# Performance work log

Hardware: AMD Instinct MI355X
Metric: run time of the kernel (lower is better)

## Reference

```python
import jax, jax.numpy as jnp
import numpy as np

STRIDES = (8, 16, 32)
INPUT = (640, 640)
NC = 80           # num_classes
CONF = 0.65       # conf_thr
IOU_THR = 0.65    # nms iou_threshold
K = 1000          # fixed candidate cap for jit-compatible NMS (padded/masked)


def _priors():
    # MlvlPointGenerator(offset=0, with_stride=True): per level, points at
    # (x*stride, y*stride) flattened y-major, format [cx, cy, stride, stride].
    ps = []
    for s in STRIDES:
        H, W = INPUT[0] // s, INPUT[1] // s
        yy, xx = jnp.meshgrid(jnp.arange(H, dtype=jnp.float32),
                              jnp.arange(W, dtype=jnp.float32), indexing='ij')
        cx = (xx * s).ravel()
        cy = (yy * s).ravel()
        st = jnp.full_like(cx, float(s))
        ps.append(jnp.stack([cx, cy, st, st], axis=-1))
    return jnp.concatenate(ps, axis=0)  # [8400, 4]


def _flatten(xs, c):
    # permute(0,2,3,1).reshape(B, -1, c) per level, concat over priors
    return jnp.concatenate(
        [x.transpose(0, 2, 3, 1).reshape(x.shape[0], -1, c) for x in xs], axis=1)


def _decode(priors, bp):
    # bp: [B, N, 4]; priors: [N, 4] (cx, cy, sw, sh)
    xys = bp[..., :2] * priors[:, 2:] + priors[:, :2]
    whs = jnp.exp(bp[..., 2:]) * priors[:, 2:]
    tl = xys - whs * 0.5
    br = xys + whs * 0.5
    return jnp.concatenate([tl, br], axis=-1)  # [B, N, 4] tlbr


def _iou(a, b):
    tl = jnp.maximum(a[:, None, :2], b[None, :, :2])
    br = jnp.minimum(a[:, None, 2:], b[None, :, 2:])
    wh = jnp.clip(br - tl, 0.0)
    inter = wh[..., 0] * wh[..., 1]
    area = lambda x: (x[:, 2] - x[:, 0]) * (x[:, 3] - x[:, 1])
    union = area(a)[:, None] + area(b)[None, :] - inter
    return inter / (union + 1e-6)


def _nms_single(cls_s, obj_s, boxes):
    # cls_s: [N, NC] sigmoid scores; obj_s: [N]; boxes: [N, 4]
    max_s = cls_s.max(axis=-1)
    labels = jnp.argmax(cls_s, axis=-1)
    score = max_s * obj_s
    valid = score >= CONF                       # confidence mask
    sc = jnp.where(valid, score, 0.0)
    top_sc, idx = jax.lax.top_k(sc, K)          # sorted descending -> greedy order
    b = boxes[idx]
    lab = labels[idx]
    v = valid[idx]
    # class-aware (batched) NMS: offset boxes per label so classes never overlap
    max_coord = jnp.max(jnp.abs(b)) + 1.0
    ob = b + (lab.astype(b.dtype) * max_coord)[:, None]
    iou = _iou(ob, ob)                          # [K, K]
    j = jnp.arange(K)
    def body(i, keep):
        sup = (iou[i] > IOU_THR) & (j > i)
        return jnp.where(keep[i] & v[i], keep & (~sup), keep)
    keep = jax.lax.fori_loop(0, K, body, jnp.ones(K, dtype=bool))
    final = keep & v
    dets = jnp.where(final[:, None],
                     jnp.concatenate([b, top_sc[:, None]], axis=-1), 0.0)  # [K, 5]
    labs = jnp.where(final, lab, -1)
    return dets, labs, final


def setup_inputs() -> dict:
    key = jax.random.key(0)
    ks = jax.random.split(key, 9)
    B = 32
    shapes = {
        'cls0': (B, NC, 80, 80), 'cls1': (B, NC, 40, 40), 'cls2': (B, NC, 20, 20),
        'bbox0': (B, 4, 80, 80), 'bbox1': (B, 4, 40, 40), 'bbox2': (B, 4, 20, 20),
        'obj0': (B, 1, 80, 80), 'obj1': (B, 1, 40, 40), 'obj2': (B, 1, 20, 20),
    }
    return {n: jax.random.normal(k, s, dtype=jnp.float32)
            for (n, s), k in zip(shapes.items(), ks)}


def reference(cls0, cls1, cls2, bbox0, bbox1, bbox2, obj0, obj1, obj2):
    priors = _priors()
    cls = jax.nn.sigmoid(_flatten([cls0, cls1, cls2], NC))       # [B, 8400, 80]
    bp = _flatten([bbox0, bbox1, bbox2], 4)                      # [B, 8400, 4]
    obj = jax.nn.sigmoid(_flatten([obj0, obj1, obj2], 1)[..., 0])  # [B, 8400]
    boxes = _decode(priors, bp)                                  # [B, 8400, 4]
    # per-image class-wise batched NMS, padded to K detections
    dets, labels, keep = jax.vmap(_nms_single)(cls, obj, boxes)
    return dets, labels, keep
```

## Files before the change

kernel.cpp:

```cpp
#include <hip/hip_runtime.h>
#include <stdint.h>

#define NPRIOR 8400
#define NB 32
#define NCLS 80
#define KTOP 1000
#define CAP 8400
#define CPAD 16

typedef unsigned long long u64;

__device__ __forceinline__ float exp_np(float x) {
#pragma clang fp contract(off)
    if (x > 88.72283935546875f) return __builtin_huge_valf();
    if (x < -87.3365478515625f) return 0.0f;
    float q = rintf(x * 1.442695040f);
    float r = fmaf(q, -6.93145752e-1f, x);
    r = fmaf(q, -1.42860677e-6f, r);
    float p = fmaf(1.9875691500e-4f, r, 1.3981999507e-3f);
    p = fmaf(p, r, 8.3334519073e-3f);
    p = fmaf(p, r, 4.1665795894e-2f);
    p = fmaf(p, r, 1.6666665459e-1f);
    p = fmaf(p, r, 5.0000001201e-1f);
    float r2 = r * r;
    p = fmaf(p, r2, r);
    p = p + 1.0f;
    return ldexpf(p, (int)q);
}
__device__ __forceinline__ float sigm_np(float x) {
#pragma clang fp contract(off)
    float t = exp_np(-x);
    return 1.0f / (1.0f + t);
}

__device__ __forceinline__ void level_of(int n, int& W, int& s, int& loc) {
    if (n < 6400)      { W = 80; s = 8;  loc = n; }
    else if (n < 8000) { W = 40; s = 16; loc = n - 6400; }
    else               { W = 20; s = 32; loc = n - 8000; }
}

__device__ float4 decode32(int b, int n,
                           const float* bb0, const float* bb1, const float* bb2) {
#pragma clang fp contract(off)
    int W, s, loc; level_of(n, W, s, loc);
    const float* bb = (s == 8) ? bb0 : (s == 16) ? bb1 : bb2;
    int hw = W * W;
    int y = loc / W, x = loc - y * W;
    const float* bp = bb + (size_t)b * 4 * hw + y * W + x;
    float fs = (float)s;
    float cx = (float)x * fs, cy = (float)y * fs;
    float xc = bp[0] * fs + cx;
    float yc = bp[hw] * fs + cy;
    float wv = exp_np(bp[2 * hw]) * fs;
    float hv = exp_np(bp[3 * hw]) * fs;
    float wv2 = wv * 0.5f, hv2 = hv * 0.5f;
    float4 r;
    r.x = xc - wv2;
    r.y = yc - hv2;
    r.z = xc + wv2;
    r.w = yc + hv2;
    return r;
}

__device__ __forceinline__ unsigned flt2ord(float f) {
    unsigned u = __float_as_uint(f);
    return u ^ ((u >> 31) ? 0xffffffffu : 0x80000000u);
}
__device__ __forceinline__ float ord2flt(unsigned u) {
    u ^= ((u >> 31) ? 0x80000000u : 0xffffffffu);
    return __uint_as_float(u);
}
__device__ __forceinline__ u64 packlc(float l, int c) {
    return ((u64)flt2ord(l) << 32) | (unsigned)(~(unsigned)c);
}

__global__ void __launch_bounds__(64) init_k(int* __restrict__ cnts_mb) {
    cnts_mb[threadIdx.x * CPAD] = 0;
}

__global__ void __launch_bounds__(256) score_k(
    const float* __restrict__ cls0, const float* __restrict__ cls1, const float* __restrict__ cls2,
    const float* __restrict__ ob0,  const float* __restrict__ ob1,  const float* __restrict__ ob2,
    float* __restrict__ sc, int* __restrict__ labels,
    u64* __restrict__ keys, int* __restrict__ cnts, int* __restrict__ rankbuf)
{
#pragma clang fp contract(off)
    int b = blockIdx.y;
    int tid = threadIdx.x, wv = tid >> 6, l = tid & 63;
    int cid = l >> 4;
    int n = blockIdx.x * 64 + wv * 16 + (l & 15);
    bool nvalid = (n < NPRIOR);
    int nc = nvalid ? n : NPRIOR - 1;
    int W, s, loc; level_of(nc, W, s, loc);
    const float* cls = (s == 8) ? cls0 : (s == 16) ? cls1 : cls2;
    const float* ob  = (s == 8) ? ob0  : (s == 16) ? ob1  : ob2;
    int hw = W * W;
    int y = loc / W, x = loc - y * W;
    const float* cp = cls + (size_t)b * NCLS * hw + y * W + x;
    int c0 = cid * 20;

    float buf[20];
#pragma unroll
    for (int k = 0; k < 20; ++k) buf[k] = cp[(size_t)(c0 + k) * hw];
    float M = buf[0], S2 = -3.4e38f;
    int I = c0;
#pragma unroll
    for (int k = 1; k < 20; ++k) {
        float lg = buf[k];
        if (lg > M) { S2 = M; M = lg; I = c0 + k; }
        else        { S2 = fmaxf(S2, lg); }
    }
    u64 p = packlc(M, I);
    float s2 = S2;
#pragma unroll
    for (int mk = 16; mk <= 32; mk <<= 1) {
        u64 po = __shfl_xor(p, mk, 64);
        float so = __shfl_xor(s2, mk, 64);
        if (po > p) { s2 = fmaxf(so, ord2flt((unsigned)(p >> 32))); p = po; }
        else        { s2 = fmaxf(s2, ord2flt((unsigned)(po >> 32))); }
    }

    float Mg = ord2flt((unsigned)(p >> 32));
    int lab = (int)(~(unsigned)(p & 0xffffffffull)) & 0xff;
    float tM = sigm_np(Mg);
    float gap = Mg - s2;
    float mx = fmaxf(fabsf(Mg), fabsf(s2));
    bool need = !((gap * exp_np(-mx)) > 1.6e-5f) && nvalid;
    if (__ballot(need)) {
        u64 pk = 0;
#pragma unroll
        for (int k = 0; k < 20; ++k) {
            float t = sigm_np(cp[(size_t)(c0 + k) * hw]);
            u64 q = ((u64)flt2ord(t) << 32) | (unsigned)(~(unsigned)(c0 + k));
            pk = (q > pk) ? q : pk;
        }
#pragma unroll
        for (int mk = 16; mk <= 32; mk <<= 1) {
            u64 qo = __shfl_xor(pk, mk, 64);
            pk = (qo > pk) ? qo : pk;
        }
        if (need) {
            tM = ord2flt((unsigned)(pk >> 32));
            lab = (int)(~(unsigned)(pk & 0xffffffffull)) & 0xff;
        }
    }

    bool owner = (cid == 0) && nvalid;
    float scv = 0.0f;
    if (owner) {
        float sObj = sigm_np(ob[(size_t)b * hw + y * W + x]);
        float score = tM * sObj;
        scv = (score >= 0.65f) ? score : 0.0f;
        sc[(size_t)b * NPRIOR + n] = scv;
        labels[(size_t)b * NPRIOR + n] = lab;
    }

    bool val = owner && (scv > 0.0f);
    u64 mb = __ballot(val);
    if (mb) {
        int lead = (int)__builtin_ctzll(mb);
        int base = 0;
        if (l == lead) base = atomicAdd(&cnts[b * CPAD], (int)__popcll(mb));
        base = __shfl(base, lead);
        if (val) {
            int pos = base + (int)__popcll(mb & ((1ull << l) - 1ull));
            keys[(size_t)b * CAP + pos] =
                ((u64)__float_as_uint(scv) << 32) | (unsigned)(~(unsigned)n);
            rankbuf[(size_t)b * CAP + pos] = 0;
        }
    }
}

__global__ void __launch_bounds__(256) rank_part(
    const u64* __restrict__ keys, const int* __restrict__ cnts,
    int* __restrict__ rankbuf)
{
    int b = blockIdx.y, tid = threadIdx.x;
    int cn = min(cnts[b * CPAD], CAP);
    int nt = (cn + 255) >> 8;
    int ntt = nt * nt;
    const u64* keyimg = keys + (size_t)b * CAP;
    int lane = tid & 63;

    for (int t = blockIdx.x; t < ntt; t += gridDim.x) {
        int it = t / nt, jt = t - it * nt;
        int i = it * 256 + tid;
        u64 ki = (i < cn) ? keyimg[i] : ~0ull;
        int rank = 0;
        int jbase = jt * 256;
        int jend = min(jbase + 256, cn);
        for (int jb = jbase; jb < jend; jb += 64) {
            int j = jb + lane;
            u64 kv = (j < cn) ? keyimg[j] : 0ull;
            unsigned lo = (unsigned)kv, hi = (unsigned)(kv >> 32);
            int lim = jend - jb;
#pragma unroll
            for (int l = 0; l < 64; ++l) {
                unsigned jlo = __builtin_amdgcn_readlane(lo, l);
                unsigned jhi = __builtin_amdgcn_readlane(hi, l);
                u64 kj = ((u64)jhi << 32) | jlo;
                rank += (l < lim && kj > ki) ? 1 : 0;
            }
        }
        if (i < cn && rank > 0) atomicAdd(&rankbuf[(size_t)b * CAP + i], rank);
    }
}

__global__ void __launch_bounds__(256) scatter_k(
    const u64* __restrict__ keys, const int* __restrict__ cnts,
    const int* __restrict__ rankbuf,
    const float* __restrict__ sc, const int* __restrict__ labels,
    const float* __restrict__ bb0, const float* __restrict__ bb1, const float* __restrict__ bb2,
    float4* __restrict__ sel_box, float* __restrict__ sel_score,
    int* __restrict__ sel_label, int* __restrict__ maxbits, u64* __restrict__ vmask)
{
#pragma clang fp contract(off)
    __shared__ float redbuf[256];
    int b = blockIdx.y, chunk = blockIdx.x, tid = threadIdx.x;
    int cn = min(cnts[b * CPAD], CAP);
    int base = chunk * 256;
    if (chunk != 0 && base >= cn) return;

    const u64* keyimg = keys + (size_t)b * CAP;
    const int* labb = labels + (size_t)b * NPRIOR;
    const float* scb = sc + (size_t)b * NPRIOR;

    int i = base + tid;
    float lmax = 0.0f;
    if (i < cn) {
        int rank = rankbuf[(size_t)b * CAP + i];
        if (rank < KTOP) {
            u64 ki = keyimg[i];
            unsigned n = ~(unsigned)(ki & 0xffffffffull);
            float s = __uint_as_float((unsigned)(ki >> 32));
            float4 bx = decode32(b, (int)n, bb0, bb1, bb2);
            sel_box[(size_t)b * 1024 + rank] = bx;
            sel_score[(size_t)b * 1024 + rank] = s;
            sel_label[(size_t)b * 1024 + rank] = labb[n];
            lmax = fmaxf(fmaxf(fabsf(bx.x), fabsf(bx.y)),
                         fmaxf(fabsf(bx.z), fabsf(bx.w)));
        }
    }

    if (chunk == 0) {
        if (cn < KTOP && tid == 0) {
            float lm = 0.0f;
            int r = cn;
            for (int n = 0; n < NPRIOR && r < KTOP; ++n) {
                if (scb[n] == 0.0f) {
                    float4 bx = decode32(b, n, bb0, bb1, bb2);
                    sel_box[(size_t)b * 1024 + r] = bx;
                    sel_score[(size_t)b * 1024 + r] = 0.0f;
                    sel_label[(size_t)b * 1024 + r] = labb[n];
                    lm = fmaxf(lm, fmaxf(fmaxf(fabsf(bx.x), fabsf(bx.y)),
                                         fmaxf(fabsf(bx.z), fabsf(bx.w))));
                    ++r;
                }
            }
            lmax = fmaxf(lmax, lm);
        }
        if (tid < 24) {
            sel_box[(size_t)b * 1024 + 1000 + tid] = make_float4(0.f, 0.f, 0.f, 0.f);
            sel_score[(size_t)b * 1024 + 1000 + tid] = 0.0f;
            sel_label[(size_t)b * 1024 + 1000 + tid] = 0;
        }
        if (tid < 16) {
            int vc = min(cn, KTOP);
            int lo = tid * 64;
            u64 m;
            if (vc >= lo + 64)      m = ~0ull;
            else if (vc <= lo)      m = 0ull;
            else                    m = (1ull << (vc - lo)) - 1ull;
            vmask[b * 16 + tid] = m;
        }
    }

    redbuf[tid] = lmax;
    __syncthreads();
    for (int off = 128; off > 0; off >>= 1) {
        if (tid < off) redbuf[tid] = fmaxf(redbuf[tid], redbuf[tid + off]);
        __syncthreads();
    }
    if (tid == 0) atomicMax(&maxbits[b * CPAD], __float_as_int(redbuf[0]));
}

__global__ void __launch_bounds__(256) build_mask_T(
    const float4* __restrict__ sel_box, const int* __restrict__ sel_label,
    const int* __restrict__ maxbits, u64* __restrict__ Cmask)
{
#pragma clang fp contract(off)
    __shared__ float4 obr[256];
    __shared__ float arr[256];
    int b = blockIdx.y;
    int cg = blockIdx.x & 15, rgq = blockIdx.x >> 4;
    if (rgq * 4 > cg) return;
    int tid = threadIdx.x, wave = tid >> 6, lane = tid & 63;
    float mc = __int_as_float(maxbits[b * CPAD]) + 1.0f;

    {
        int row = rgq * 256 + tid;
        float4 v = sel_box[(size_t)b * 1024 + row];
        float off = (float)sel_label[(size_t)b * 1024 + row] * mc;
        v.x += off; v.y += off; v.z += off; v.w += off;
        obr[tid] = v;
        arr[tid] = (v.z - v.x) * (v.w - v.y);
    }
    int col = cg * 64 + lane;
    float4 a = sel_box[(size_t)b * 1024 + col];
    float offc = (float)sel_label[(size_t)b * 1024 + col] * mc;
    a.x += offc; a.y += offc; a.z += offc; a.w += offc;
    float ac = (a.z - a.x) * (a.w - a.y);
    __syncthreads();

    int rg = rgq * 4 + wave;
    if (rg > cg) return;
    u64 bits = 0;
    int rowbase = rg * 64;
#pragma unroll 8
    for (int r = 0; r < 64; ++r) {
        int row = rowbase + r;
        float4 rb = obr[wave * 64 + r];
        float ra = arr[wave * 64 + r];
        bool pred = false;
        if (row < col && row < KTOP && col < KTOP) {
            float tlx = fmaxf(rb.x, a.x), tly = fmaxf(rb.y, a.y);
            float brx = fminf(rb.z, a.z), bry = fminf(rb.w, a.w);
            float w = fmaxf(brx - tlx, 0.0f), h = fmaxf(bry - tly, 0.0f);
            float inter = w * h;
            float uni = (ra + ac) - inter;
            float iou = inter / (uni + 1e-6f);
            pred = iou > 0.65f;
        }
        bits |= pred ? (1ull << r) : 0ull;
    }
    Cmask[((size_t)b * 16 + rg) * 1024 + col] = bits;
}

__global__ void __launch_bounds__(64) nms_fixpoint_write(
    const u64* __restrict__ Cmask, const u64* __restrict__ vmask,
    const float4* __restrict__ sel_box, const float* __restrict__ sel_score,
    const int* __restrict__ sel_label, float* __restrict__ out)
{
    int b = blockIdx.x, lane = threadIdx.x;
    const u64* Cimg = Cmask + (size_t)b * 16 * 1024;
    u64 Khist[16];
#pragma unroll
    for (int g = 0; g < 16; ++g) {
        int col = g * 64 + lane;
        bool supp = false;
#pragma unroll
        for (int gp = 0; gp < g; ++gp)
            supp |= (Cimg[(size_t)gp * 1024 + col] & Khist[gp]) != 0ull;
        u64 V = vmask[b * 16 + g] & ~__ballot(supp);
        u64 T = Cimg[(size_t)g * 1024 + col];
        u64 K = V;
        for (int it = 0; it < 64; ++it) {
            u64 Knew = V & ~__ballot((T & K) != 0ull);
            if (Knew == K) break;
            K = Knew;
        }
        Khist[g] = K;
    }

    const size_t selo = (size_t)b * 1024;
    float* lab_o = out + (size_t)NB * KTOP * 5;
    float* keep_o = lab_o + (size_t)NB * KTOP;
#pragma unroll
    for (int g = 0; g < 16; ++g) {
        int k = g * 64 + lane;
        if (k >= KTOP) break;
        bool fin = (Khist[g] >> lane) & 1ull;
        float4 bx = sel_box[selo + k];
        float s = sel_score[selo + k];
        int lb = sel_label[selo + k];
        size_t o5 = ((size_t)b * KTOP + k) * 5;
        out[o5 + 0] = fin ? bx.x : 0.0f;
        out[o5 + 1] = fin ? bx.y : 0.0f;
        out[o5 + 2] = fin ? bx.z : 0.0f;
        out[o5 + 3] = fin ? bx.w : 0.0f;
        out[o5 + 4] = fin ? s : 0.0f;
        lab_o[b * KTOP + k] = fin ? (float)lb : -1.0f;
        keep_o[b * KTOP + k] = fin ? 1.0f : 0.0f;
    }
}

extern "C" void kernel_launch(void* const* d_in, const int* in_sizes, int n_in,
                              void* d_out, int out_size, void* d_ws, size_t ws_size,
                              hipStream_t stream) {
    const float* cls0 = (const float*)d_in[0];
    const float* cls1 = (const float*)d_in[1];
    const float* cls2 = (const float*)d_in[2];
    const float* bb0  = (const float*)d_in[3];
    const float* bb1  = (const float*)d_in[4];
    const float* bb2  = (const float*)d_in[5];
    const float* ob0  = (const float*)d_in[6];
    const float* ob1  = (const float*)d_in[7];
    const float* ob2  = (const float*)d_in[8];
    float* out = (float*)d_out;

    char* w = (char*)d_ws;
    size_t used = 0;
    auto alloc = [&](size_t bytes) -> void* {
        void* p = (void*)(w + used);
        used += (bytes + 255) & ~(size_t)255;
        return p;
    };
    float* sc        = (float*)alloc((size_t)NB * NPRIOR * 4);
    int* labels      = (int*)alloc((size_t)NB * NPRIOR * 4);
    u64* keys        = (u64*)alloc((size_t)NB * CAP * 8);
    int* cnts_mb     = (int*)alloc((size_t)2 * NB * CPAD * 4);
    int* rankbuf     = (int*)alloc((size_t)NB * CAP * 4);
    float4* sel_box  = (float4*)alloc((size_t)NB * 1024 * 16);
    float* sel_score = (float*)alloc((size_t)NB * 1024 * 4);
    int* sel_label   = (int*)alloc((size_t)NB * 1024 * 4);
    u64* vmask       = (u64*)alloc((size_t)NB * 16 * 8);
    u64* Cmask       = (u64*)alloc((size_t)NB * 16 * 1024 * 8);

    if (used > ws_size) return;

    int* cnts = cnts_mb;
    int* maxbits = cnts_mb + NB * CPAD;

    init_k<<<1, 64, 0, stream>>>(cnts_mb);
    score_k<<<dim3((NPRIOR + 63) / 64, NB), 256, 0, stream>>>(
        cls0, cls1, cls2, ob0, ob1, ob2, sc, labels, keys, cnts, rankbuf);
    rank_part<<<dim3(64, NB), 256, 0, stream>>>(keys, cnts, rankbuf);
    scatter_k<<<dim3((CAP + 255) / 256, NB), 256, 0, stream>>>(
        keys, cnts, rankbuf, sc, labels, bb0, bb1, bb2,
        sel_box, sel_score, sel_label, maxbits, vmask);
    build_mask_T<<<dim3(64, NB), 256, 0, stream>>>(sel_box, sel_label, maxbits, Cmask);
    nms_fixpoint_write<<<NB, 64, 0, stream>>>(
        Cmask, vmask, sel_box, sel_score, sel_label, out);
}
```

Before: 117.4 us.

## Fuse rank, scatter, mask-build and NMS into one persistent kernel with grid barriers

Replaces four separate kernel launches (rank, scatter, IoU mask build, fixpoint NMS) with a single persistent kernel of 512 blocks that loops over the work items of each stage and uses software grid-wide barriers between stages. The init kernel is replaced by a hipMemsetAsync that also zeroes the barrier counters. This removes launch gaps and per-kernel tail effects. In exchange it relies on all 512 blocks being co-resident, since a spin barrier otherwise deadlocks or times out, and the final NMS stage runs on only 32 blocks while the rest sit idle.

Result: slower. 345.1 us (+193.8%).

```diff
diff --git a/kernel.cpp b/kernel.cpp
--- a/kernel.cpp
+++ b/kernel.cpp
@@ -7,6 +7,7 @@
 #define KTOP 1000
 #define CAP 8400
 #define CPAD 16
+#define FBLK 512
 
 typedef unsigned long long u64;
 
@@ -74,10 +75,6 @@
     return ((u64)flt2ord(l) << 32) | (unsigned)(~(unsigned)c);
 }
 
-__global__ void __launch_bounds__(64) init_k(int* __restrict__ cnts_mb) {
-    cnts_mb[threadIdx.x * CPAD] = 0;
-}
-
 __global__ void __launch_bounds__(256) score_k(
     const float* __restrict__ cls0, const float* __restrict__ cls1, const float* __restrict__ cls2,
     const float* __restrict__ ob0,  const float* __restrict__ ob1,  const float* __restrict__ ob2,
@@ -171,216 +168,233 @@
     }
 }
 
-__global__ void __launch_bounds__(256) rank_part(
-    const u64* __restrict__ keys, const int* __restrict__ cnts,
-    int* __restrict__ rankbuf)
-{
-    int b = blockIdx.y, tid = threadIdx.x;
-    int cn = min(cnts[b * CPAD], CAP);
-    int nt = (cn + 255) >> 8;
-    int ntt = nt * nt;
-    const u64* keyimg = keys + (size_t)b * CAP;
-    int lane = tid & 63;
-
-    for (int t = blockIdx.x; t < ntt; t += gridDim.x) {
-        int it = t / nt, jt = t - it * nt;
-        int i = it * 256 + tid;
-        u64 ki = (i < cn) ? keyimg[i] : ~0ull;
-        int rank = 0;
-        int jbase = jt * 256;
-        int jend = min(jbase + 256, cn);
-        for (int jb = jbase; jb < jend; jb += 64) {
-            int j = jb + lane;
-            u64 kv = (j < cn) ? keyimg[j] : 0ull;
-            unsigned lo = (unsigned)kv, hi = (unsigned)(kv >> 32);
-            int lim = jend - jb;
-#pragma unroll
-            for (int l = 0; l < 64; ++l) {
-                unsigned jlo = __builtin_amdgcn_readlane(lo, l);
-                unsigned jhi = __builtin_amdgcn_readlane(hi, l);
-                u64 kj = ((u64)jhi << 32) | jlo;
-                rank += (l < lim && kj > ki) ? 1 : 0;
-            }
-        }
-        if (i < cn && rank > 0) atomicAdd(&rankbuf[(size_t)b * CAP + i], rank);
-    }
-}
-
-__global__ void __launch_bounds__(256) scatter_k(
-    const u64* __restrict__ keys, const int* __restrict__ cnts,
-    const int* __restrict__ rankbuf,
+__device__ __forceinline__ void gridbar(int* bar, int slot) {
+    __syncthreads();
+    if (threadIdx.x == 0) {
+        __threadfence();
+        int* cnt = bar + slot * 2;
+        int* rel = bar + slot * 2 + 1;
+        int prev = __hip_atomic_fetch_add(cnt, 1, __ATOMIC_ACQ_REL, __HIP_MEMORY_SCOPE_AGENT);
+        if (prev == FBLK - 1) {
+            __hip_atomic_store(rel, 1, __ATOMIC_RELEASE, __HIP_MEMORY_SCOPE_AGENT);
+        } else {
+            long spins = 0;
+            while (__hip_atomic_load(rel, __ATOMIC_ACQUIRE, __HIP_MEMORY_SCOPE_AGENT) == 0) {
+                if (++spins > 300000000L) break;
+                __builtin_amdgcn_s_sleep(8);
+            }
+        }
+        __threadfence();
+    }
+    __syncthreads();
+}
+
+__global__ void __launch_bounds__(256, 4) fused_k(
+    const u64* __restrict__ keys, int* __restrict__ cnts,
+    int* __restrict__ rankbuf,
     const float* __restrict__ sc, const int* __restrict__ labels,
     const float* __restrict__ bb0, const float* __restrict__ bb1, const float* __restrict__ bb2,
     float4* __restrict__ sel_box, float* __restrict__ sel_score,
-    int* __restrict__ sel_label, int* __restrict__ maxbits, u64* __restrict__ vmask)
-{
-#pragma clang fp contract(off)
-    __shared__ float redbuf[256];
-    int b = blockIdx.y, chunk = blockIdx.x, tid = threadIdx.x;
-    int cn = min(cnts[b * CPAD], CAP);
-    int base = chunk * 256;
-    if (chunk != 0 && base >= cn) return;
-
-    const u64* keyimg = keys + (size_t)b * CAP;
-    const int* labb = labels + (size_t)b * NPRIOR;
-    const float* scb = sc + (size_t)b * NPRIOR;
-
-    int i = base + tid;
-    float lmax = 0.0f;
-    if (i < cn) {
-        int rank = rankbuf[(size_t)b * CAP + i];
-        if (rank < KTOP) {
-            u64 ki = keyimg[i];
-            unsigned n = ~(unsigned)(ki & 0xffffffffull);
-            float s = __uint_as_float((unsigned)(ki >> 32));
-            float4 bx = decode32(b, (int)n, bb0, bb1, bb2);
-            sel_box[(size_t)b * 1024 + rank] = bx;
-            sel_score[(size_t)b * 1024 + rank] = s;
-            sel_label[(size_t)b * 1024 + rank] = labb[n];
-            lmax = fmaxf(fmaxf(fabsf(bx.x), fabsf(bx.y)),
-                         fmaxf(fabsf(bx.z), fabsf(bx.w)));
-        }
-    }
-
-    if (chunk == 0) {
-        if (cn < KTOP && tid == 0) {
-            float lm = 0.0f;
-            int r = cn;
-            for (int n = 0; n < NPRIOR && r < KTOP; ++n) {
-                if (scb[n] == 0.0f) {
-                    float4 bx = decode32(b, n, bb0, bb1, bb2);
-                    sel_box[(size_t)b * 1024 + r] = bx;
-                    sel_score[(size_t)b * 1024 + r] = 0.0f;
-                    sel_label[(size_t)b * 1024 + r] = labb[n];
-                    lm = fmaxf(lm, fmaxf(fmaxf(fabsf(bx.x), fabsf(bx.y)),
-                                         fmaxf(fabsf(bx.z), fabsf(bx.w))));
-                    ++r;
-                }
-            }
-            lmax = fmaxf(lmax, lm);
-        }
-        if (tid < 24) {
-            sel_box[(size_t)b * 1024 + 1000 + tid] = make_float4(0.f, 0.f, 0.f, 0.f);
-            sel_score[(size_t)b * 1024 + 1000 + tid] = 0.0f;
-            sel_label[(size_t)b * 1024 + 1000 + tid] = 0;
-        }
-        if (tid < 16) {
-            int vc = min(cn, KTOP);
-            int lo = tid * 64;
-            u64 m;
-            if (vc >= lo + 64)      m = ~0ull;
-            else if (vc <= lo)      m = 0ull;
-            else                    m = (1ull << (vc - lo)) - 1ull;
-            vmask[b * 16 + tid] = m;
-        }
-    }
-
-    redbuf[tid] = lmax;
-    __syncthreads();
-    for (int off = 128; off > 0; off >>= 1) {
-        if (tid < off) redbuf[tid] = fmaxf(redbuf[tid], redbuf[tid + off]);
-        __syncthreads();
-    }
-    if (tid == 0) atomicMax(&maxbits[b * CPAD], __float_as_int(redbuf[0]));
-}
-
-__global__ void __launch_bounds__(256) build_mask_T(
-    const float4* __restrict__ sel_box, const int* __restrict__ sel_label,
-    const int* __restrict__ maxbits, u64* __restrict__ Cmask)
+    int* __restrict__ sel_label, int* __restrict__ maxbits, u64* __restrict__ vmask,
+    u64* __restrict__ Cmask, float* __restrict__ out, int* __restrict__ bar)
 {
 #pragma clang fp contract(off)
     __shared__ float4 obr[256];
     __shared__ float arr[256];
-    int b = blockIdx.y;
-    int cg = blockIdx.x & 15, rgq = blockIdx.x >> 4;
-    if (rgq * 4 > cg) return;
-    int tid = threadIdx.x, wave = tid >> 6, lane = tid & 63;
-    float mc = __int_as_float(maxbits[b * CPAD]) + 1.0f;
-
-    {
-        int row = rgq * 256 + tid;
-        float4 v = sel_box[(size_t)b * 1024 + row];
-        float off = (float)sel_label[(size_t)b * 1024 + row] * mc;
-        v.x += off; v.y += off; v.z += off; v.w += off;
-        obr[tid] = v;
-        arr[tid] = (v.z - v.x) * (v.w - v.y);
-    }
-    int col = cg * 64 + lane;
-    float4 a = sel_box[(size_t)b * 1024 + col];
-    float offc = (float)sel_label[(size_t)b * 1024 + col] * mc;
-    a.x += offc; a.y += offc; a.z += offc; a.w += offc;
-    float ac = (a.z - a.x) * (a.w - a.y);
-    __syncthreads();
-
-    int rg = rgq * 4 + wave;
-    if (rg > cg) return;
-    u64 bits = 0;
-    int rowbase = rg * 64;
+    __shared__ float redbuf[256];
+    int blk = blockIdx.x, tid = threadIdx.x, lane = tid & 63;
+
+    for (int j = blk; j < NB * 64; j += FBLK) {
+        int b = j >> 6, slot = j & 63;
+        int cn = min(cnts[b * CPAD], CAP);
+        int nt = (cn + 255) >> 8;
+        int ntt = nt * nt;
+        const u64* keyimg = keys + (size_t)b * CAP;
+        for (int t = slot; t < ntt; t += 64) {
+            int it = t / nt, jt = t - it * nt;
+            int i = it * 256 + tid;
+            u64 ki = (i < cn) ? keyimg[i] : ~0ull;
+            int rank = 0;
+            int jbase = jt * 256;
+            int jend = min(jbase + 256, cn);
+            for (int jb = jbase; jb < jend; jb += 64) {
+                int jj = jb + lane;
+                u64 kv = (jj < cn) ? keyimg[jj] : 0ull;
+                unsigned lo = (unsigned)kv, hi = (unsigned)(kv >> 32);
+                int lim = jend - jb;
+#pragma unroll
+                for (int l2 = 0; l2 < 64; ++l2) {
+                    unsigned jlo = __builtin_amdgcn_readlane(lo, l2);
+                    unsigned jhi = __builtin_amdgcn_readlane(hi, l2);
+                    u64 kj = ((u64)jhi << 32) | jlo;
+                    rank += (l2 < lim && kj > ki) ? 1 : 0;
+                }
+            }
+            if (i < cn && rank > 0) atomicAdd(&rankbuf[(size_t)b * CAP + i], rank);
+        }
+    }
+    gridbar(bar, 0);
+
+    for (int j = blk; j < NB * 33; j += FBLK) {
+        int b = j / 33, chunk = j - b * 33;
+        int cn = min(cnts[b * CPAD], CAP);
+        int base = chunk * 256;
+        if (chunk != 0 && base >= cn) continue;
+
+        const u64* keyimg = keys + (size_t)b * CAP;
+        const int* labb = labels + (size_t)b * NPRIOR;
+        const float* scb = sc + (size_t)b * NPRIOR;
+
+        int i = base + tid;
+        float lmax = 0.0f;
+        if (i < cn) {
+            int rank = rankbuf[(size_t)b * CAP + i];
+            if (rank < KTOP) {
+                u64 ki = keyimg[i];
+                unsigned n = ~(unsigned)(ki & 0xffffffffull);
+                float s = __uint_as_float((unsigned)(ki >> 32));
+                float4 bx = decode32(b, (int)n, bb0, bb1, bb2);
+                sel_box[(size_t)b * 1024 + rank] = bx;
+                sel_score[(size_t)b * 1024 + rank] = s;
+                sel_label[(size_t)b * 1024 + rank] = labb[n];
+                lmax = fmaxf(fmaxf(fabsf(bx.x), fabsf(bx.y)),
+                             fmaxf(fabsf(bx.z), fabsf(bx.w)));
+            }
+        }
+        if (chunk == 0) {
+            if (cn < KTOP && tid == 0) {
+                float lm = 0.0f;
+                int r = cn;
+                for (int n = 0; n < NPRIOR && r < KTOP; ++n) {
+                    if (scb[n] == 0.0f) {
+                        float4 bx = decode32(b, n, bb0, bb1, bb2);
+                        sel_box[(size_t)b * 1024 + r] = bx;
+                        sel_score[(size_t)b * 1024 + r] = 0.0f;
+                        sel_label[(size_t)b * 1024 + r] = labb[n];
+                        lm = fmaxf(lm, fmaxf(fmaxf(fabsf(bx.x), fabsf(bx.y)),
+                                             fmaxf(fabsf(bx.z), fabsf(bx.w))));
+                        ++r;
+                    }
+                }
+                lmax = fmaxf(lmax, lm);
+            }
+            if (tid < 24) {
+                sel_box[(size_t)b * 1024 + 1000 + tid] = make_float4(0.f, 0.f, 0.f, 0.f);
+                sel_score[(size_t)b * 1024 + 1000 + tid] = 0.0f;
+                sel_label[(size_t)b * 1024 + 1000 + tid] = 0;
+            }
+            if (tid < 16) {
+                int vc = min(cn, KTOP);
+                int lo = tid * 64;
+                u64 m;
+                if (vc >= lo + 64)      m = ~0ull;
+                else if (vc <= lo)      m = 0ull;
+                else                    m = (1ull << (vc - lo)) - 1ull;
+                vmask[b * 16 + tid] = m;
+            }
+        }
+        __syncthreads();
+        redbuf[tid] = lmax;
+        __syncthreads();
+        for (int off = 128; off > 0; off >>= 1) {
+            if (tid < off) redbuf[tid] = fmaxf(redbuf[tid], redbuf[tid + off]);
+            __syncthreads();
+        }
+        if (tid == 0) atomicMax(&maxbits[b * CPAD], __float_as_int(redbuf[0]));
+    }
+    gridbar(bar, 1);
+
+    for (int j = blk; j < NB * 64; j += FBLK) {
+        int b = j >> 6, xx = j & 63;
+        int cg = xx & 15, rgq = xx >> 4;
+        if (rgq * 4 > cg) continue;
+        int wave = tid >> 6;
+        float mc = __int_as_float(
+            __hip_atomic_load(&maxbits[b * CPAD], __ATOMIC_RELAXED,
+                              __HIP_MEMORY_SCOPE_AGENT)) + 1.0f;
+        __syncthreads();
+        {
+            int row = rgq * 256 + tid;
+            float4 v = sel_box[(size_t)b * 1024 + row];
+            float off = (float)sel_label[(size_t)b * 1024 + row] * mc;
+            v.x += off; v.y += off; v.z += off; v.w += off;
+            obr[tid] = v;
+            arr[tid] = (v.z - v.x) * (v.w - v.y);
+        }
+        int col = cg * 64 + lane;
+        float4 a = sel_box[(size_t)b * 1024 + col];
+        float offc = (float)sel_label[(size_t)b * 1024 + col] * mc;
+        a.x += offc; a.y += offc; a.z += offc; a.w += offc;
+        float ac = (a.z - a.x) * (a.w - a.y);
+        __syncthreads();
+
+        int rg = rgq * 4 + wave;
+        if (rg <= cg) {
+            u64 bits = 0;
+            int rowbase = rg * 64;
 #pragma unroll 8
-    for (int r = 0; r < 64; ++r) {
-        int row = rowbase + r;
-        float4 rb = obr[wave * 64 + r];
-        float ra = arr[wave * 64 + r];
-        bool pred = false;
-        if (row < col && row < KTOP && col < KTOP) {
-            float tlx = fmaxf(rb.x, a.x), tly = fmaxf(rb.y, a.y);
-            float brx = fminf(rb.z, a.z), bry = fminf(rb.w, a.w);
-            float w = fmaxf(brx - tlx, 0.0f), h = fmaxf(bry - tly, 0.0f);
-            float inter = w * h;
-            float uni = (ra + ac) - inter;
-            float iou = inter / (uni + 1e-6f);
-            pred = iou > 0.65f;
-        }
-        bits |= pred ? (1ull << r) : 0ull;
-    }
-    Cmask[((size_t)b * 16 + rg) * 1024 + col] = bits;
-}
-
-__global__ void __launch_bounds__(64) nms_fixpoint_write(
-    const u64* __restrict__ Cmask, const u64* __restrict__ vmask,
-    const float4* __restrict__ sel_box, const float* __restrict__ sel_score,
-    const int* __restrict__ sel_label, float* __restrict__ out)
-{
-    int b = blockIdx.x, lane = threadIdx.x;
-    const u64* Cimg = Cmask + (size_t)b * 16 * 1024;
-    u64 Khist[16];
-#pragma unroll
-    for (int g = 0; g < 16; ++g) {
-        int col = g * 64 + lane;
-        bool supp = false;
-#pragma unroll
-        for (int gp = 0; gp < g; ++gp)
-            supp |= (Cimg[(size_t)gp * 1024 + col] & Khist[gp]) != 0ull;
-        u64 V = vmask[b * 16 + g] & ~__ballot(supp);
-        u64 T = Cimg[(size_t)g * 1024 + col];
-        u64 K = V;
-        for (int it = 0; it < 64; ++it) {
-            u64 Knew = V & ~__ballot((T & K) != 0ull);
-            if (Knew == K) break;
-            K = Knew;
-        }
-        Khist[g] = K;
-    }
-
-    const size_t selo = (size_t)b * 1024;
-    float* lab_o = out + (size_t)NB * KTOP * 5;
-    float* keep_o = lab_o + (size_t)NB * KTOP;
-#pragma unroll
-    for (int g = 0; g < 16; ++g) {
-        int k = g * 64 + lane;
-        if (k >= KTOP) break;
-        bool fin = (Khist[g] >> lane) & 1ull;
-        float4 bx = sel_box[selo + k];
-        float s = sel_score[selo + k];
-        int lb = sel_label[selo + k];
-        size_t o5 = ((size_t)b * KTOP + k) * 5;
-        out[o5 + 0] = fin ? bx.x : 0.0f;
-        out[o5 + 1] = fin ? bx.y : 0.0f;
-        out[o5 + 2] = fin ? bx.z : 0.0f;
-        out[o5 + 3] = fin ? bx.w : 0.0f;
-        out[o5 + 4] = fin ? s : 0.0f;
-        lab_o[b * KTOP + k] = fin ? (float)lb : -1.0f;
-        keep_o[b * KTOP + k] = fin ? 1.0f : 0.0f;
+            for (int r = 0; r < 64; ++r) {
+                int row = rowbase + r;
+                float4 rb = obr[wave * 64 + r];
+                float ra = arr[wave * 64 + r];
+                bool pred = false;
+                if (row < col && row < KTOP && col < KTOP) {
+                    float tlx = fmaxf(rb.x, a.x), tly = fmaxf(rb.y, a.y);
+                    float brx = fminf(rb.z, a.z), bry = fminf(rb.w, a.w);
+                    float w2 = fmaxf(brx - tlx, 0.0f), h2 = fmaxf(bry - tly, 0.0f);
+                    float inter = w2 * h2;
+                    float uni = (ra + ac) - inter;
+                    float iou = inter / (uni + 1e-6f);
+                    pred = iou > 0.65f;
+                }
+                bits |= pred ? (1ull << r) : 0ull;
+            }
+            Cmask[((size_t)b * 16 + rg) * 1024 + col] = bits;
+        }
+    }
+    gridbar(bar, 2);
+
+    if (blk < NB && tid < 64) {
+        int b = blk;
+        const u64* Cimg = Cmask + (size_t)b * 16 * 1024;
+        u64 Khist[16];
+#pragma unroll
+        for (int g = 0; g < 16; ++g) {
+            int col = g * 64 + lane;
+            bool supp = false;
+#pragma unroll
+            for (int gp = 0; gp < g; ++gp)
+                supp |= (Cimg[(size_t)gp * 1024 + col] & Khist[gp]) != 0ull;
+            u64 V = vmask[b * 16 + g] & ~__ballot(supp);
+            u64 T = Cimg[(size_t)g * 1024 + col];
+            u64 K = V;
+            for (int it = 0; it < 64; ++it) {
+                u64 Knew = V & ~__ballot((T & K) != 0ull);
+                if (Knew == K) break;
+                K = Knew;
+            }
+            Khist[g] = K;
+        }
+        const size_t selo = (size_t)b * 1024;
+        float* lab_o = out + (size_t)NB * KTOP * 5;
+        float* keep_o = lab_o + (size_t)NB * KTOP;
+#pragma unroll
+        for (int g = 0; g < 16; ++g) {
+            int k = g * 64 + lane;
+            if (k >= KTOP) break;
+            bool fin = (Khist[g] >> lane) & 1ull;
+            float4 bx = sel_box[selo + k];
+            float s = sel_score[selo + k];
+            int lb = sel_label[selo + k];
+            size_t o5 = ((size_t)b * KTOP + k) * 5;
+            out[o5 + 0] = fin ? bx.x : 0.0f;
+            out[o5 + 1] = fin ? bx.y : 0.0f;
+            out[o5 + 2] = fin ? bx.z : 0.0f;
+            out[o5 + 3] = fin ? bx.w : 0.0f;
+            out[o5 + 4] = fin ? s : 0.0f;
+            lab_o[b * KTOP + k] = fin ? (float)lb : -1.0f;
+            keep_o[b * KTOP + k] = fin ? 1.0f : 0.0f;
+        }
     }
 }
 
@@ -405,10 +419,10 @@
         used += (bytes + 255) & ~(size_t)255;
         return p;
     };
+    int* zeroed      = (int*)alloc((size_t)(2 * NB * CPAD + 16) * 4);
     float* sc        = (float*)alloc((size_t)NB * NPRIOR * 4);
     int* labels      = (int*)alloc((size_t)NB * NPRIOR * 4);
     u64* keys        = (u64*)alloc((size_t)NB * CAP * 8);
-    int* cnts_mb     = (int*)alloc((size_t)2 * NB * CPAD * 4);
     int* rankbuf     = (int*)alloc((size_t)NB * CAP * 4);
     float4* sel_box  = (float4*)alloc((size_t)NB * 1024 * 16);
     float* sel_score = (float*)alloc((size_t)NB * 1024 * 4);
@@ -418,17 +432,14 @@
 
     if (used > ws_size) return;
 
-    int* cnts = cnts_mb;
-    int* maxbits = cnts_mb + NB * CPAD;
-
-    init_k<<<1, 64, 0, stream>>>(cnts_mb);
+    int* cnts = zeroed;
+    int* maxbits = zeroed + NB * CPAD;
+    int* bar = zeroed + 2 * NB * CPAD;
+
+    hipMemsetAsync(zeroed, 0, (size_t)(2 * NB * CPAD + 16) * 4, stream);
     score_k<<<dim3((NPRIOR + 63) / 64, NB), 256, 0, stream>>>(
         cls0, cls1, cls2, ob0, ob1, ob2, sc, labels, keys, cnts, rankbuf);
-    rank_part<<<dim3(64, NB), 256, 0, stream>>>(keys, cnts, rankbuf);
-    scatter_k<<<dim3((CAP + 255) / 256, NB), 256, 0, stream>>>(
+    fused_k<<<FBLK, 256, 0, stream>>>(
         keys, cnts, rankbuf, sc, labels, bb0, bb1, bb2,
-        sel_box, sel_score, sel_label, maxbits, vmask);
-    build_mask_T<<<dim3(64, NB), 256, 0, stream>>>(sel_box, sel_label, maxbits, Cmask);
-    nms_fixpoint_write<<<NB, 64, 0, stream>>>(
-        Cmask, vmask, sel_box, sel_score, sel_label, out);
-}
+        sel_box, sel_score, sel_label, maxbits, vmask, Cmask, out, bar);
+}
```
